# Kernel tuning notes

Hardware: AMD Instinct MI355X
Metric: run time of the kernel (lower is better)

## Reference

```python
import jax, jax.numpy as jnp
import numpy as np

SIGMAS = [15, 80, 250]  # hardcoded defaults in retinex_MSR


def _gauss_k1d(sigma):
    # matches get_gauss_kernel(sigma, dim=1)
    ksize = int(np.floor(sigma * 6) / 2) * 2 + 1
    k = np.arange(ksize, dtype=np.float32) - ksize // 2
    k = np.exp(-k ** 2 / (2.0 * sigma ** 2))
    k /= k.sum()
    return jnp.asarray(k)


def _gauss_blur(x, k1d):
    # x: (N, 1, H, W); separable blur with zero padding, same as F.conv2d
    K = k1d.shape[0]
    pad = K // 2
    dn = ('NCHW', 'OIHW', 'NCHW')
    kv = k1d.reshape(1, 1, K, 1)
    kh = k1d.reshape(1, 1, 1, K)
    x = jax.lax.conv_general_dilated(x, kv, (1, 1), [(pad, pad), (0, 0)], dimension_numbers=dn)
    x = jax.lax.conv_general_dilated(x, kh, (1, 1), [(0, 0), (pad, pad)], dimension_numbers=dn)
    return x


def setup_inputs() -> dict:
    key = jax.random.key(0)
    img = jax.random.uniform(key, (16, 3, 512, 512), dtype=jnp.float32)
    return {"img": img}


def reference(img):
    B, C, H, W = img.shape
    # all channels processed identically as single-channel depthwise convs:
    # fold channels into batch for one big conv per sigma
    x = img.astype(jnp.float32).reshape(B * C, 1, H, W)
    w = 1.0 / len(SIGMAS)  # default equal weights summing to 1
    r = jnp.zeros((B * C, 1, H, W), dtype=jnp.float32)
    for sigma in SIGMAS:
        r = r + jnp.log(_gauss_blur(x, _gauss_k1d(sigma)) + 1.0) * w
    r = r.reshape(B, C, H, W)
    # per-channel min-max stretch, global over batch and spatial dims
    mmin = r.min(axis=(0, 2, 3), keepdims=True)
    mmax = r.max(axis=(0, 2, 3), keepdims=True)
    return (r - mmin) / (mmax - mmin)
```

## Files before the change

kernel.cpp:

```cpp
#include <hip/hip_runtime.h>
#include <math.h>


#define NSL 48

#define W0_OFF 0
#define W1_OFF 512
#define W2_OFF 1280
#define MM_OFF 2816
#define G16_BYTE_OFF 16384
#define X16_BYTE_OFF 1589248
#define T16_BYTE_OFF 26755072

typedef _Float16 half8 __attribute__((ext_vector_type(8)));
typedef float f32x4 __attribute__((ext_vector_type(4)));

__device__ __forceinline__ void gload16(const void* g, void* l) {
  __builtin_amdgcn_global_load_lds(
      (const __attribute__((address_space(1))) void*)g,
      (__attribute__((address_space(3))) void*)l, 16, 0, 0);
}

__global__ void wkern(float* __restrict__ ws) {
  __shared__ float red[256];
  const int s = blockIdx.x;
  const int Ks[3] = {91, 481, 1501};
  const float sg[3] = {15.f, 80.f, 250.f};
  const int off[3] = {W0_OFF, W1_OFF, W2_OFF};
  const int alloc[3] = {512, 768, 1536};
  const int K = Ks[s], A = alloc[s];
  float* wb = ws + off[s];
  const int t = threadIdx.x;
  for (int i = t; i < A; i += 256) wb[i] = 0.f;
  __syncthreads();
  const float inv2s2 = 1.f / (2.f * sg[s] * sg[s]);
  float part = 0.f;
  for (int i = t; i < K; i += 256) {
    const float d = (float)(i - K / 2);
    const float e = __expf(-d * d * inv2s2);
    wb[16 + i] = e;
    part += e;
  }
  red[t] = part;
  __syncthreads();
  for (int st = 128; st > 0; st >>= 1) {
    if (t < st) red[t] += red[t + st];
    __syncthreads();
  }
  const float inv = 1.f / red[0];
  for (int i = t; i < K; i += 256) wb[16 + i] *= inv;
}

__global__ void mm_init(unsigned* __restrict__ mm) {
  const int t = threadIdx.x;
  if (t < 3) mm[t] = 0xFFFFFFFFu;
  else if (t < 6) mm[t] = 0u;
}

__global__ void gkern(const float* __restrict__ ws, _Float16* __restrict__ gb) {
  const int y = blockIdx.x;
  const int s = blockIdx.y;
  const int Rs[3] = {45, 240, 750};
  const int off[3] = {W0_OFF, W1_OFF, W2_OFF};
  const float* w = ws + off[s] + 16;
  _Float16* g = gb + ((size_t)s << 18) + ((size_t)y << 9);
  const int R = Rs[s], K = 2 * R + 1;
  for (int x = threadIdx.x; x < 512; x += 256) {
    const int i = x - y + R;
    const float v = (i >= 0 && i < K) ? w[i] : 0.f;
    g[x] = (_Float16)v;
  }
}

__global__ __launch_bounds__(256) void xconv(const float* __restrict__ X,
                                             _Float16* __restrict__ X16) {
  const size_t i = ((size_t)blockIdx.x * 256 + threadIdx.x) << 3;
  const float4 v0 = *reinterpret_cast<const float4*>(X + i);
  const float4 v1 = *reinterpret_cast<const float4*>(X + i + 4);
  half8 h;
  h[0] = (_Float16)v0.x; h[1] = (_Float16)v0.y;
  h[2] = (_Float16)v0.z; h[3] = (_Float16)v0.w;
  h[4] = (_Float16)v1.x; h[5] = (_Float16)v1.y;
  h[6] = (_Float16)v1.z; h[7] = (_Float16)v1.w;
  *reinterpret_cast<half8*>(X16 + i) = h;
}

#define STAGE(buf, k0)                                                              \
  do {                                                                              \
    _Pragma("unroll") for (int q = 0; q < 2; ++q) {                                 \
      const int idx = (q << 8) + t;                                                 \
      const int row = idx >> 2;                                                     \
      const int c8 = (idx & 3) << 3;                                                \
      gload16(Ap + ((size_t)(bm + row) << 9) + (k0) + c8, &As[buf][idx << 3]);      \
      gload16(Bp + ((size_t)(bn + row) << 9) + (k0) + c8, &Bs[buf][idx << 3]);      \
    }                                                                               \
  } while (0)

#define FRAGS_AND_MFMA(buf)                                                         \
  do {                                                                              \
    half8 af[4], bf[4];                                                             \
    _Pragma("unroll") for (int f = 0; f < 4; ++f) {                                 \
      af[f] = *reinterpret_cast<const half8*>(                                      \
          &As[buf][(((wr << 6) + (f << 4) + lr) << 5) + (lg << 3)]);                \
      bf[f] = *reinterpret_cast<const half8*>(                                      \
          &Bs[buf][(((wc << 6) + (f << 4) + lr) << 5) + (lg << 3)]);                \
    }                                                                               \
    _Pragma("unroll") for (int fm = 0; fm < 4; ++fm)                                \
        _Pragma("unroll") for (int fn = 0; fn < 4; ++fn)                            \
        acc[fm][fn] = __builtin_amdgcn_mfma_f32_16x16x32_f16(af[fm], bf[fn],        \
                                                             acc[fm][fn], 0, 0, 0); \
  } while (0)

__global__ __launch_bounds__(256) void gemm1_k(const _Float16* __restrict__ X16,
                                               const _Float16* __restrict__ G16,
                                               _Float16* __restrict__ T16) {
  __shared__ __align__(16) _Float16 As[2][128 * 32];
  __shared__ __align__(16) _Float16 Bs[2][128 * 32];
  const int t = threadIdx.x;
  const int lane = t & 63, wave = t >> 6;
  const int wr = wave >> 1, wc = wave & 1;
  const int lr = lane & 15, lg = lane >> 4;
  const int bn = blockIdx.x << 7;
  const int bm = blockIdx.y << 7;
  const int z = blockIdx.z;
  const int s = z / NSL;
  const int slice = z - s * NSL;
  const int Rs[3] = {45, 240, 750};
  const int R = Rs[s];
  const _Float16* Ap = G16 + ((size_t)s << 18);
  const _Float16* Bp = X16 + ((size_t)slice << 18);
  _Float16* Tout = T16 + ((size_t)z << 18);

  int klo = bm - R;
  klo = (klo > 0 ? klo : 0) >> 5;
  int khi = bm + 127 + R;
  if (khi > 511) khi = 511;
  khi >>= 5;

  f32x4 acc[4][4];
#pragma unroll
  for (int i = 0; i < 4; ++i)
#pragma unroll
    for (int j = 0; j < 4; ++j) acc[i][j] = (f32x4){0.f, 0.f, 0.f, 0.f};

  int cur = 0;
  STAGE(0, klo << 5);
  __syncthreads();
  for (int kt = klo; kt <= khi; ++kt) {
    if (kt < khi) STAGE(cur ^ 1, (kt + 1) << 5);
    FRAGS_AND_MFMA(cur);
    __syncthreads();
    cur ^= 1;
  }

#pragma unroll
  for (int fm = 0; fm < 4; ++fm)
#pragma unroll
    for (int fn = 0; fn < 4; ++fn) {
      const int a0 = bm + (wr << 6) + (fm << 4) + (lg << 2);
      const int b0 = bn + (wc << 6) + (fn << 4) + lr;
#pragma unroll
      for (int j = 0; j < 4; ++j)
        Tout[((size_t)(a0 + j) << 9) + b0] = (_Float16)acc[fm][fn][j];
    }
}

__global__ __launch_bounds__(256) void gemm2_k(const _Float16* __restrict__ G16,
                                               const _Float16* __restrict__ T16,
                                               float* __restrict__ out,
                                               unsigned* __restrict__ mm) {
  __shared__ __align__(16) _Float16 As[2][128 * 32];
  __shared__ __align__(16) _Float16 Bs[2][128 * 32];
  __shared__ float smn[4], smx[4];
  const int t = threadIdx.x;
  const int lane = t & 63, wave = t >> 6;
  const int wr = wave >> 1, wc = wave & 1;
  const int lr = lane & 15, lg = lane >> 4;
  const int bn = blockIdx.x << 7;
  const int bm = blockIdx.y << 7;
  const int slice = blockIdx.z;
  const float w3 = 1.f / 3.f;
  const int Rs[3] = {45, 240, 750};

  f32x4 res[4][4];
#pragma unroll
  for (int i = 0; i < 4; ++i)
#pragma unroll
    for (int j = 0; j < 4; ++j) res[i][j] = (f32x4){0.f, 0.f, 0.f, 0.f};

  int cur = 0;
#pragma unroll 1
  for (int s = 0; s < 3; ++s) {
    const int R = Rs[s];
    const _Float16* Ap = G16 + ((size_t)s << 18);
    const _Float16* Bp = T16 + ((size_t)(s * NSL + slice) << 18);
    int klo = bm - R;
    klo = (klo > 0 ? klo : 0) >> 5;
    int khi = bm + 127 + R;
    if (khi > 511) khi = 511;
    khi >>= 5;

    f32x4 acc[4][4];
#pragma unroll
    for (int i = 0; i < 4; ++i)
#pragma unroll
      for (int j = 0; j < 4; ++j) acc[i][j] = (f32x4){0.f, 0.f, 0.f, 0.f};

    STAGE(cur, klo << 5);
    __syncthreads();
    for (int kt = klo; kt <= khi; ++kt) {
      if (kt < khi) STAGE(cur ^ 1, (kt + 1) << 5);
      FRAGS_AND_MFMA(cur);
      __syncthreads();
      cur ^= 1;
    }

#pragma unroll
    for (int fm = 0; fm < 4; ++fm)
#pragma unroll
      for (int fn = 0; fn < 4; ++fn)
#pragma unroll
        for (int j = 0; j < 4; ++j)
          res[fm][fn][j] += w3 * __logf(acc[fm][fn][j] + 1.f);
  }

  float mn = 3.4e38f, mx = -3.4e38f;
#pragma unroll
  for (int fm = 0; fm < 4; ++fm)
#pragma unroll
    for (int fn = 0; fn < 4; ++fn) {
      const int rb = bm + (wr << 6) + (fm << 4) + (lg << 2);
      const int cg = bn + (wc << 6) + (fn << 4) + lr;
      float* op = out + ((size_t)slice << 18) + ((size_t)rb << 9) + cg;
#pragma unroll
      for (int j = 0; j < 4; ++j) {
        const float v = res[fm][fn][j];
        op[j << 9] = v;
        mn = fminf(mn, v);
        mx = fmaxf(mx, v);
      }
    }
#pragma unroll
  for (int off = 32; off > 0; off >>= 1) {
    mn = fminf(mn, __shfl_xor(mn, off));
    mx = fmaxf(mx, __shfl_xor(mx, off));
  }
  if (lane == 0) {
    smn[wave] = mn;
    smx[wave] = mx;
  }
  __syncthreads();
  if (t == 0) {
    mn = fminf(fminf(smn[0], smn[1]), fminf(smn[2], smn[3]));
    mx = fmaxf(fmaxf(smx[0], smx[1]), fmaxf(smx[2], smx[3]));
    const int ch = slice % 3;
    atomicMin(&mm[ch], __float_as_uint(mn));
    atomicMax(&mm[3 + ch], __float_as_uint(mx));
  }
}

__global__ __launch_bounds__(256) void norm_k(float* __restrict__ r,
                                              const unsigned* __restrict__ mm) {
  const int b = blockIdx.x;
  const int slice = b >> 4;
  const int piece = b & 15;
  const int ch = slice % 3;
  const float mn = __uint_as_float(mm[ch]);
  const float mx = __uint_as_float(mm[3 + ch]);
  const float inv = 1.f / (mx - mn);
  float* p = r + ((size_t)slice << 18) + (piece << 14);
  const int t = threadIdx.x;
  for (int q = 0; q < 16; ++q) {
    float4 v = *reinterpret_cast<const float4*>(&p[(q * 256 + t) << 2]);
    v.x = (v.x - mn) * inv;
    v.y = (v.y - mn) * inv;
    v.z = (v.z - mn) * inv;
    v.w = (v.w - mn) * inv;
    *reinterpret_cast<float4*>(&p[(q * 256 + t) << 2]) = v;
  }
}

extern "C" void kernel_launch(void* const* d_in, const int* in_sizes, int n_in,
                              void* d_out, int out_size, void* d_ws, size_t ws_size,
                              hipStream_t stream) {
  const float* img = (const float*)d_in[0];
  float* out = (float*)d_out;
  float* wsf = (float*)d_ws;
  unsigned* mm = (unsigned*)(wsf + MM_OFF);
  _Float16* G16 = (_Float16*)((char*)d_ws + G16_BYTE_OFF);
  _Float16* X16 = (_Float16*)((char*)d_ws + X16_BYTE_OFF);
  _Float16* T16 = (_Float16*)((char*)d_ws + T16_BYTE_OFF);

  wkern<<<3, 256, 0, stream>>>(wsf);
  mm_init<<<1, 64, 0, stream>>>(mm);
  gkern<<<dim3(512, 3), 256, 0, stream>>>(wsf, G16);
  xconv<<<6144, 256, 0, stream>>>(img, X16);

  gemm1_k<<<dim3(4, 4, 3 * NSL), 256, 0, stream>>>(X16, G16, T16);
  gemm2_k<<<dim3(4, 4, NSL), 256, 0, stream>>>(G16, T16, out, mm);

  norm_k<<<768, 256, 0, stream>>>(out, mm);
}
```

Measured before the change: 163.2 us.

## Triple-buffer LDS staging with vmcnt waits and single barrier per k-step

Replaces the double-buffered K loop in both banded GEMM kernels with a three-stage pipeline. Loads are issued two tiles ahead via global_load_lds, and a partial s_waitcnt vmcnt(4) plus one s_barrier per iteration replaces the two __syncthreads. The intent is to hide global-to-LDS latency and cut synchronisation. It raises LDS use to 48KB per block, which may lower occupancy, and it depends on STAGE issuing exactly 4 loads per thread for the wait count to be correct.

```diff
diff --git a/kernel.cpp b/kernel.cpp
--- a/kernel.cpp
+++ b/kernel.cpp
@@ -20,6 +20,11 @@
       (const __attribute__((address_space(1))) void*)g,
       (__attribute__((address_space(3))) void*)l, 16, 0, 0);
 }
+
+#define WAITV4() asm volatile("s_waitcnt vmcnt(4)" ::: "memory")
+#define WAITV0() asm volatile("s_waitcnt vmcnt(0)" ::: "memory")
+#define SCHEDB() __builtin_amdgcn_sched_barrier(0)
+#define BARRIER() __builtin_amdgcn_s_barrier()
 
 __global__ void wkern(float* __restrict__ ws) {
   __shared__ float red[256];
@@ -111,11 +116,30 @@
                                                              acc[fm][fn], 0, 0, 0); \
   } while (0)
 
+#define K_PIPELINE_LOOP()                                                           \
+  do {                                                                              \
+    STAGE(0, klo << 5);                                                             \
+    STAGE(1, (klo + 1) << 5);                                                       \
+    int cb = 0;                                                                     \
+    for (int kt = klo; kt <= khi; ++kt) {                                           \
+      if (kt < khi) { WAITV4(); } else { WAITV0(); }                                \
+      SCHEDB();                                                                     \
+      BARRIER();                                                                    \
+      SCHEDB();                                                                     \
+      if (kt + 2 <= khi) {                                                          \
+        const int sb = (cb + 2 >= 3) ? cb - 1 : cb + 2;                             \
+        STAGE(sb, (kt + 2) << 5);                                                   \
+      }                                                                             \
+      FRAGS_AND_MFMA(cb);                                                           \
+      cb = (cb == 2) ? 0 : cb + 1;                                                  \
+    }                                                                               \
+  } while (0)
+
 __global__ __launch_bounds__(256) void gemm1_k(const _Float16* __restrict__ X16,
                                                const _Float16* __restrict__ G16,
                                                _Float16* __restrict__ T16) {
-  __shared__ __align__(16) _Float16 As[2][128 * 32];
-  __shared__ __align__(16) _Float16 Bs[2][128 * 32];
+  __shared__ __align__(16) _Float16 As[3][128 * 32];
+  __shared__ __align__(16) _Float16 Bs[3][128 * 32];
   const int t = threadIdx.x;
   const int lane = t & 63, wave = t >> 6;
   const int wr = wave >> 1, wc = wave & 1;
@@ -143,15 +167,7 @@
 #pragma unroll
     for (int j = 0; j < 4; ++j) acc[i][j] = (f32x4){0.f, 0.f, 0.f, 0.f};
 
-  int cur = 0;
-  STAGE(0, klo << 5);
-  __syncthreads();
-  for (int kt = klo; kt <= khi; ++kt) {
-    if (kt < khi) STAGE(cur ^ 1, (kt + 1) << 5);
-    FRAGS_AND_MFMA(cur);
-    __syncthreads();
-    cur ^= 1;
-  }
+  K_PIPELINE_LOOP();
 
 #pragma unroll
   for (int fm = 0; fm < 4; ++fm)
@@ -169,8 +185,8 @@
                                                const _Float16* __restrict__ T16,
                                                float* __restrict__ out,
                                                unsigned* __restrict__ mm) {
-  __shared__ __align__(16) _Float16 As[2][128 * 32];
-  __shared__ __align__(16) _Float16 Bs[2][128 * 32];
+  __shared__ __align__(16) _Float16 As[3][128 * 32];
+  __shared__ __align__(16) _Float16 Bs[3][128 * 32];
   __shared__ float smn[4], smx[4];
   const int t = threadIdx.x;
   const int lane = t & 63, wave = t >> 6;
@@ -188,7 +204,6 @@
 #pragma unroll
     for (int j = 0; j < 4; ++j) res[i][j] = (f32x4){0.f, 0.f, 0.f, 0.f};
 
-  int cur = 0;
 #pragma unroll 1
   for (int s = 0; s < 3; ++s) {
     const int R = Rs[s];
@@ -206,14 +221,8 @@
 #pragma unroll
       for (int j = 0; j < 4; ++j) acc[i][j] = (f32x4){0.f, 0.f, 0.f, 0.f};
 
-    STAGE(cur, klo << 5);
-    __syncthreads();
-    for (int kt = klo; kt <= khi; ++kt) {
-      if (kt < khi) STAGE(cur ^ 1, (kt + 1) << 5);
-      FRAGS_AND_MFMA(cur);
-      __syncthreads();
-      cur ^= 1;
-    }
+    BARRIER();
+    K_PIPELINE_LOOP();
 
 #pragma unroll
     for (int fm = 0; fm < 4; ++fm)
```

After: 161.9 us. No clear change (-0.8%).

## Load MFMA fragments directly from global into registers, dropping LDS staging

Applied to the files above, without the earlier changes.

Both banded GEMM kernels now load the A/B half8 fragments straight from global memory into registers, ping-ponging two fragment sets. This replaces the LDS double buffer and its per-tile __syncthreads. The goal is to cut LDS traffic and barrier stalls and to let waves run independently, with launch_bounds raised to request two blocks per CU. In exchange each wave re-reads data that other waves in the block share, so global/L2 traffic rises. The strided 16-byte row loads may also coalesce poorly, and register pressure goes up.

```diff
diff --git a/kernel.cpp b/kernel.cpp
--- a/kernel.cpp
+++ b/kernel.cpp
@@ -15,11 +15,10 @@
 typedef _Float16 half8 __attribute__((ext_vector_type(8)));
 typedef float f32x4 __attribute__((ext_vector_type(4)));
 
-__device__ __forceinline__ void gload16(const void* g, void* l) {
-  __builtin_amdgcn_global_load_lds(
-      (const __attribute__((address_space(1))) void*)g,
-      (__attribute__((address_space(3))) void*)l, 16, 0, 0);
-}
+struct Frags {
+  half8 a[4];
+  half8 b[4];
+};
 
 __global__ void wkern(float* __restrict__ ws) {
   __shared__ float red[256];
@@ -85,37 +84,42 @@
   *reinterpret_cast<half8*>(X16 + i) = h;
 }
 
-#define STAGE(buf, k0)                                                              \
-  do {                                                                              \
-    _Pragma("unroll") for (int q = 0; q < 2; ++q) {                                 \
-      const int idx = (q << 8) + t;                                                 \
-      const int row = idx >> 2;                                                     \
-      const int c8 = (idx & 3) << 3;                                                \
-      gload16(Ap + ((size_t)(bm + row) << 9) + (k0) + c8, &As[buf][idx << 3]);      \
-      gload16(Bp + ((size_t)(bn + row) << 9) + (k0) + c8, &Bs[buf][idx << 3]);      \
-    }                                                                               \
+#define LOADSET(S, kt_)                                                           \
+  do {                                                                            \
+    _Pragma("unroll") for (int f = 0; f < 4; ++f) {                               \
+      S.a[f] = *reinterpret_cast<const half8*>(aptr + ((size_t)(kt_) << 5) +      \
+                                               (f << 13));                        \
+      S.b[f] = *reinterpret_cast<const half8*>(bptr + ((size_t)(kt_) << 5) +      \
+                                               (f << 13));                        \
+    }                                                                             \
   } while (0)
 
-#define FRAGS_AND_MFMA(buf)                                                         \
-  do {                                                                              \
-    half8 af[4], bf[4];                                                             \
-    _Pragma("unroll") for (int f = 0; f < 4; ++f) {                                 \
-      af[f] = *reinterpret_cast<const half8*>(                                      \
-          &As[buf][(((wr << 6) + (f << 4) + lr) << 5) + (lg << 3)]);                \
-      bf[f] = *reinterpret_cast<const half8*>(                                      \
-          &Bs[buf][(((wc << 6) + (f << 4) + lr) << 5) + (lg << 3)]);                \
-    }                                                                               \
-    _Pragma("unroll") for (int fm = 0; fm < 4; ++fm)                                \
-        _Pragma("unroll") for (int fn = 0; fn < 4; ++fn)                            \
-        acc[fm][fn] = __builtin_amdgcn_mfma_f32_16x16x32_f16(af[fm], bf[fn],        \
+#define MFMASET(S)                                                                \
+  do {                                                                            \
+    _Pragma("unroll") for (int fm = 0; fm < 4; ++fm)                              \
+        _Pragma("unroll") for (int fn = 0; fn < 4; ++fn)                          \
+        acc[fm][fn] = __builtin_amdgcn_mfma_f32_16x16x32_f16(S.a[fm], S.b[fn],    \
                                                              acc[fm][fn], 0, 0, 0); \
   } while (0)
 
-__global__ __launch_bounds__(256) void gemm1_k(const _Float16* __restrict__ X16,
-                                               const _Float16* __restrict__ G16,
-                                               _Float16* __restrict__ T16) {
-  __shared__ __align__(16) _Float16 As[2][128 * 32];
-  __shared__ __align__(16) _Float16 Bs[2][128 * 32];
+#define K_REG_LOOP()                                                              \
+  do {                                                                            \
+    Frags fA, fB;                                                                 \
+    LOADSET(fA, klo);                                                             \
+    int kt = klo;                                                                 \
+    while (kt + 1 <= khi) {                                                       \
+      LOADSET(fB, kt + 1);                                                        \
+      MFMASET(fA);                                                                \
+      if (kt + 2 <= khi) LOADSET(fA, kt + 2);                                     \
+      MFMASET(fB);                                                                \
+      kt += 2;                                                                    \
+    }                                                                             \
+    if (kt <= khi) MFMASET(fA);                                                   \
+  } while (0)
+
+__global__ __launch_bounds__(256, 2) void gemm1_k(const _Float16* __restrict__ X16,
+                                                  const _Float16* __restrict__ G16,
+                                                  _Float16* __restrict__ T16) {
   const int t = threadIdx.x;
   const int lane = t & 63, wave = t >> 6;
   const int wr = wave >> 1, wc = wave & 1;
@@ -137,21 +141,16 @@
   if (khi > 511) khi = 511;
   khi >>= 5;
 
+  const _Float16* aptr = Ap + ((size_t)(bm + (wr << 6) + lr) << 9) + (lg << 3);
+  const _Float16* bptr = Bp + ((size_t)(bn + (wc << 6) + lr) << 9) + (lg << 3);
+
   f32x4 acc[4][4];
 #pragma unroll
   for (int i = 0; i < 4; ++i)
 #pragma unroll
     for (int j = 0; j < 4; ++j) acc[i][j] = (f32x4){0.f, 0.f, 0.f, 0.f};
 
-  int cur = 0;
-  STAGE(0, klo << 5);
-  __syncthreads();
-  for (int kt = klo; kt <= khi; ++kt) {
-    if (kt < khi) STAGE(cur ^ 1, (kt + 1) << 5);
-    FRAGS_AND_MFMA(cur);
-    __syncthreads();
-    cur ^= 1;
-  }
+  K_REG_LOOP();
 
 #pragma unroll
   for (int fm = 0; fm < 4; ++fm)
@@ -165,12 +164,10 @@
     }
 }
 
-__global__ __launch_bounds__(256) void gemm2_k(const _Float16* __restrict__ G16,
-                                               const _Float16* __restrict__ T16,
-                                               float* __restrict__ out,
-                                               unsigned* __restrict__ mm) {
-  __shared__ __align__(16) _Float16 As[2][128 * 32];
-  __shared__ __align__(16) _Float16 Bs[2][128 * 32];
+__global__ __launch_bounds__(256, 2) void gemm2_k(const _Float16* __restrict__ G16,
+                                                  const _Float16* __restrict__ T16,
+                                                  float* __restrict__ out,
+                                                  unsigned* __restrict__ mm) {
   __shared__ float smn[4], smx[4];
   const int t = threadIdx.x;
   const int lane = t & 63, wave = t >> 6;
@@ -188,7 +185,6 @@
 #pragma unroll
     for (int j = 0; j < 4; ++j) res[i][j] = (f32x4){0.f, 0.f, 0.f, 0.f};
 
-  int cur = 0;
 #pragma unroll 1
   for (int s = 0; s < 3; ++s) {
     const int R = Rs[s];
@@ -200,20 +196,16 @@
     if (khi > 511) khi = 511;
     khi >>= 5;
 
+    const _Float16* aptr = Ap + ((size_t)(bm + (wr << 6) + lr) << 9) + (lg << 3);
+    const _Float16* bptr = Bp + ((size_t)(bn + (wc << 6) + lr) << 9) + (lg << 3);
+
     f32x4 acc[4][4];
 #pragma unroll
     for (int i = 0; i < 4; ++i)
 #pragma unroll
       for (int j = 0; j < 4; ++j) acc[i][j] = (f32x4){0.f, 0.f, 0.f, 0.f};
 
-    STAGE(cur, klo << 5);
-    __syncthreads();
-    for (int kt = klo; kt <= khi; ++kt) {
-      if (kt < khi) STAGE(cur ^ 1, (kt + 1) << 5);
-      FRAGS_AND_MFMA(cur);
-      __syncthreads();
-      cur ^= 1;
-    }
+    K_REG_LOOP();
 
 #pragma unroll
     for (int fm = 0; fm < 4; ++fm)
```

New measurement: 271.7 us. +66.5%, slower.
